# Kernel tuning notes

Measured on AMD Instinct MI355X. Metric: run time of the kernel, lower is better.

## Reference

```python
import jax, jax.numpy as jnp
import numpy as np

NEG_MAX = -jnp.finfo(jnp.float32).max


def apply_rotary(x):
    # x: (b, h, n, d) with d = key_dim; interleaved rotary (lucidrains rotary-embedding-torch)
    d = x.shape[-1]
    n = x.shape[-2]
    inv_freq = 1.0 / (10000.0 ** (jnp.arange(0, d, 2, dtype=jnp.float32) / d))
    t = jnp.arange(n, dtype=jnp.float32)
    freqs = t[:, None] * inv_freq[None, :]              # (n, d/2)
    cos, sin = jnp.cos(freqs), jnp.sin(freqs)
    x1, x2 = x[..., 0::2], x[..., 1::2]                 # even/odd interleaved pairs
    out1 = x1 * cos - x2 * sin
    out2 = x1 * sin + x2 * cos
    return jnp.stack([out1, out2], axis=-1).reshape(x.shape)


def setup_inputs() -> dict:
    key = jax.random.key(0)
    ks = jax.random.split(key, 12)
    b, n, dim, de = 2, 1024, 256, 64
    h, kd, vd = 8, 32, 32
    node_in = jax.random.normal(ks[0], (b, n, dim), dtype=jnp.float32)
    edge_in = jax.random.normal(ks[1], (b, n, n, de), dtype=jnp.float32)
    mask = jax.random.randint(ks[2], (b, n), 0, 2).astype(bool)
    s = 1.0 / np.sqrt(dim)
    Wq = jax.random.normal(ks[3], (dim, h * kd), dtype=jnp.float32) * s
    Wk = jax.random.normal(ks[4], (dim, h * kd), dtype=jnp.float32) * s
    Wv = jax.random.normal(ks[5], (dim, h * vd), dtype=jnp.float32) * s
    We = jax.random.normal(ks[6], (de, h), dtype=jnp.float32) * (1.0 / np.sqrt(de))
    be = jax.random.normal(ks[7], (h,), dtype=jnp.float32) * 0.01
    Wo = jax.random.normal(ks[8], (h * (vd + de), dim), dtype=jnp.float32) * (1.0 / np.sqrt(h * (vd + de)))
    bo = jax.random.normal(ks[9], (dim,), dtype=jnp.float32) * 0.01
    return {"node_in": node_in, "edge_in": edge_in, "mask": mask,
            "Wq": Wq, "Wk": Wk, "Wv": Wv, "We": We, "be": be, "Wo": Wo, "bo": bo}


def reference(node_in, edge_in, mask, Wq, Wk, Wv, We, be, Wo, bo):
    b, n, dim = node_in.shape
    h = be.shape[0]
    kd = Wq.shape[1] // h
    vd = Wv.shape[1] // h
    num_attn_logits = 2
    node_scale = (num_attn_logits * kd) ** -0.5
    edge_scale = num_attn_logits ** -0.5

    # projections -> (b, h, n, d)
    def proj(W, d):
        return (node_in @ W).reshape(b, n, h, d).transpose(0, 2, 1, 3)
    q, k, v = proj(Wq, kd), proj(Wk, kd), proj(Wv, vd)
    q, k = apply_rotary(q), apply_rotary(k)

    logits = jnp.einsum('bhid,bhjd->bhij', q, k) * node_scale
    edge_bias = (jnp.einsum('bijd,dh->bijh', edge_in, We) + be)  # (b, n, n, h)
    logits = logits + edge_bias.transpose(0, 3, 1, 2) * edge_scale

    pair_mask = mask[:, :, None] & mask[:, None, :]              # (b, n, n)
    logits = jnp.where(pair_mask[:, None, :, :], logits, NEG_MAX)

    attn = jax.nn.softmax(logits, axis=-1)                       # (b, h, n, n)

    res_node = jnp.einsum('bhij,bhjd->bhid', attn, v)            # (b, h, n, vd)
    res_edge = jnp.einsum('bhij,bijd->bhid', attn, edge_in)      # (b, h, n, de)

    res_node = res_node.transpose(0, 2, 1, 3).reshape(b, n, h * vd)
    res_edge = res_edge.transpose(0, 2, 1, 3).reshape(b, n, -1)
    out = jnp.concatenate([res_node, res_edge], axis=-1) @ Wo + bo
    return out
```

## Files before the change

kernel.cpp:

```cpp
#include <hip/hip_runtime.h>
#include <hip/hip_bf16.h>

typedef float f32x4 __attribute__((ext_vector_type(4)));
typedef short short8 __attribute__((ext_vector_type(8)));
typedef unsigned short u16;
typedef unsigned int u32;
typedef unsigned int u32x4 __attribute__((ext_vector_type(4)));
typedef unsigned short u16x8 __attribute__((ext_vector_type(8)));

#define NEG_MAX (-3.4028234663852886e38f)
#define NODE_SCALE 0.125f
#define EDGE_SCALE 0.70710678118654752f
#define TSTR 68
#define QSTR 36

__device__ __forceinline__ float bf2f(u16 u) {
  unsigned int w = ((unsigned int)u) << 16;
  return __builtin_bit_cast(float, w);
}
__device__ __forceinline__ u16 f2bf(float f) {
  unsigned int x = __builtin_bit_cast(unsigned int, f);
  x = x + 0x7FFFu + ((x >> 16) & 1u);
  return (u16)(x >> 16);
}
__device__ __forceinline__ float asf(u32 x) { return __builtin_bit_cast(float, x); }
__device__ __forceinline__ u32 cvtpk(float lo, float hi) {
  u32 r;
  asm("v_cvt_pk_bf16_f32 %0, %1, %2" : "=v"(r) : "v"(lo), "v"(hi));
  return r;
}

__global__ void mask_norm(const unsigned char* __restrict__ mraw,
                          float* __restrict__ mask_f) {
  __shared__ int flags;
  int t = threadIdx.x;
  if (t == 0) flags = 0;
  __syncthreads();
  const unsigned int* mu = (const unsigned int*)mraw;
  int f = 0;
  for (int e = t; e < 512; e += 256) { if (mu[e] > 1u) f |= 1; }
  for (int e = t; e < 2048; e += 256) { if (mraw[e] > 1) f |= 2; }
  if (f) atomicOr(&flags, f);
  __syncthreads();
  int fl = flags;
  for (int e = t; e < 2048; e += 256) {
    float v;
    if (!(fl & 1))      v = (mu[e] != 0u) ? 1.f : 0.f;
    else if (!(fl & 2)) v = (mraw[e] != 0) ? 1.f : 0.f;
    else                v = (((const float*)mraw)[e] != 0.f) ? 1.f : 0.f;
    mask_f[e] = v;
  }
}

__global__ __launch_bounds__(256) void qkv_rope(
    const float* __restrict__ node, const float* __restrict__ Wq,
    const float* __restrict__ Wk, const float* __restrict__ Wv,
    float* __restrict__ qw, u16* __restrict__ kwb, u16* __restrict__ vwb) {
  __shared__ __align__(16) float xs[8 * 256];
  int t = threadIdx.x;
  int row0 = blockIdx.x * 8;
#pragma unroll
  for (int p = 0; p < 2; ++p) {
    int f = p * 256 + t;
    *(f32x4*)(&xs[f * 4]) = *(const f32x4*)(node + (size_t)row0 * 256 + f * 4);
  }
  __syncthreads();
  float qa[8], ka[8], va[8];
#pragma unroll
  for (int r = 0; r < 8; ++r) { qa[r] = 0.f; ka[r] = 0.f; va[r] = 0.f; }
  for (int c = 0; c < 256; ++c) {
    float wq = Wq[c * 256 + t];
    float wk = Wk[c * 256 + t];
    float wv = Wv[c * 256 + t];
#pragma unroll
    for (int r = 0; r < 8; ++r) {
      float x = xs[r * 256 + c];
      qa[r] += x * wq; ka[r] += x * wk; va[r] += x * wv;
    }
  }
  int d = t & 31;
  float inv = powf(10000.f, -((float)(2 * (d >> 1)) * (1.f / 32.f)));
  int h = t >> 5;
#pragma unroll
  for (int r = 0; r < 8; ++r) {
    int gr = row0 + r;
    int b = gr >> 10, i = gr & 1023;
    float ang = (float)i * inv;
    float sn, cs;
    sincosf(ang, &sn, &cs);
    float qp = __shfl_xor(qa[r], 1, 64);
    float kp = __shfl_xor(ka[r], 1, 64);
    float qo = (d & 1) ? (qp * sn + qa[r] * cs) : (qa[r] * cs - qp * sn);
    float ko = (d & 1) ? (kp * sn + ka[r] * cs) : (ka[r] * cs - kp * sn);
    int idx = ((b * 8 + h) * 1024 + i) * 32 + d;
    qw[idx] = qo;
    kwb[idx] = f2bf(ko);
    vwb[idx] = f2bf(va[r]);
  }
}

#define WREG 1704
__global__ __launch_bounds__(256) void attn_fused(
    const float* __restrict__ edge, const float* __restrict__ qw,
    const u16* __restrict__ kwb, const u16* __restrict__ vwb,
    const float* __restrict__ We, const float* __restrict__ be,
    const float* __restrict__ mask_f, float* __restrict__ rescat) {
  __shared__ __align__(16) float S[4 * WREG];

  int bid = blockIdx.x;
  int xcd = bid & 7, slot = bid >> 3;
  int b = xcd >> 2;
  int i = (xcd & 3) * 256 + slot;
  int t = threadIdx.x;
  int lane = t & 63;
  int w = __builtin_amdgcn_readfirstlane(t >> 6);

  float* tile = S + w * WREG;
  float* Pf = tile + 1088;
  float* Bg = Pf + 160;
  float* qsw = Bg + 160;
  float* Rg = qsw + 288;

  int hg = lane >> 4, jl = lane & 15;
  int hD = lane >> 3, sD = lane & 7;
  int jrl = lane >> 2, c4 = lane & 3;
  int jh = sD >> 2, do4 = sD & 3;

  float mi = mask_f[b * 1024 + i];
  u32 mb = 0;
  if (mi != 0.f) {
#pragma unroll
    for (int tt = 0; tt < 16; ++tt) {
      float v = mask_f[b * 1024 + tt * 64 + w * 16 + jl];
      mb |= (v != 0.f ? 1u : 0u) << tt;
    }
  }
  float bes1 = be[hg] * EDGE_SCALE, bes2 = be[hg + 4] * EDGE_SCALE;

  {
    int qh = lane >> 3, qd = (lane & 7) * 4;
    f32x4 qv = *(const f32x4*)(qw + ((size_t)((b * 8 + qh) * 1024 + i)) * 32 + qd);
    *(f32x4*)(qsw + qh * QSTR + qd) = qv;
  }

  short8 weA0, weA1;
  {
    int hh = lane & 15, g = lane >> 4;
#pragma unroll
    for (int e = 0; e < 8; ++e) {
      int d0 = g * 8 + e;
      float w0 = (hh < 8) ? We[d0 * 8 + hh] * EDGE_SCALE : 0.f;
      float w1 = (hh < 8) ? We[(d0 + 32) * 8 + hh] * EDGE_SCALE : 0.f;
      weA0[e] = (short)f2bf(w0);
      weA1[e] = (short)f2bf(w1);
    }
  }

  const float* ebase = edge + ((size_t)(b * 1024 + i)) * (1024 * 64);
  const float* gsrc = ebase + (size_t)(w * 16 + jrl) * 64 + c4 * 16;
  float* wdst = tile + jrl * TSTR + c4 * 16;

  {
    f32x4 a0 = __builtin_nontemporal_load((const f32x4*)(gsrc + 0));
    f32x4 a1 = __builtin_nontemporal_load((const f32x4*)(gsrc + 4));
    f32x4 a2 = __builtin_nontemporal_load((const f32x4*)(gsrc + 8));
    f32x4 a3 = __builtin_nontemporal_load((const f32x4*)(gsrc + 12));
    *(f32x4*)(wdst + 0) = a0;
    *(f32x4*)(wdst + 4) = a1;
    *(f32x4*)(wdst + 8) = a2;
    *(f32x4*)(wdst + 12) = a3;
  }

  float m1 = NEG_MAX, m2 = NEG_MAX, s1 = 0.f, s2 = 0.f;
  f32x4 av0 = {0.f, 0.f, 0.f, 0.f}, av1 = {0.f, 0.f, 0.f, 0.f};
  f32x4 ae0 = {0.f, 0.f, 0.f, 0.f}, ae1 = {0.f, 0.f, 0.f, 0.f};

  for (int tt = 0; tt < 16; ++tt) {
    int j0 = tt * 64;
    bool pf = tt < 15;
    f32x4 st0, st1, st2, st3;
    if (pf) {
      const float* g = gsrc + (size_t)(j0 + 64) * 64;
      st0 = __builtin_nontemporal_load((const f32x4*)(g + 0));
      st1 = __builtin_nontemporal_load((const f32x4*)(g + 4));
      st2 = __builtin_nontemporal_load((const f32x4*)(g + 8));
      st3 = __builtin_nontemporal_load((const f32x4*)(g + 12));
    }
    int jg = j0 + w * 16 + jl;
    const u16* kr1 = kwb + ((size_t)((b * 8 + hg) * 1024 + jg)) * 32;
    const u16* kr2 = kwb + ((size_t)((b * 8 + hg + 4) * 1024 + jg)) * 32;
    u32x4 k1[4], k2[4];
#pragma unroll
    for (int g = 0; g < 4; ++g) {
      k1[g] = *(const u32x4*)(kr1 + g * 8);
      k2[g] = *(const u32x4*)(kr2 + g * 8);
    }
    {
      const float* rp = tile + jl * TSTR + hg * 8;
      f32x4 ea0 = *(const f32x4*)(rp + 0);
      f32x4 ea1 = *(const f32x4*)(rp + 4);
      f32x4 eb0 = *(const f32x4*)(rp + 32);
      f32x4 eb1 = *(const f32x4*)(rp + 36);
      u32x4 p0, p1;
      p0[0] = cvtpk(ea0.x, ea0.y); p0[1] = cvtpk(ea0.z, ea0.w);
      p0[2] = cvtpk(ea1.x, ea1.y); p0[3] = cvtpk(ea1.z, ea1.w);
      p1[0] = cvtpk(eb0.x, eb0.y); p1[1] = cvtpk(eb0.z, eb0.w);
      p1[2] = cvtpk(eb1.x, eb1.y); p1[3] = cvtpk(eb1.z, eb1.w);
      short8 bf0 = __builtin_bit_cast(short8, p0);
      short8 bf1 = __builtin_bit_cast(short8, p1);
      f32x4 bacc = {0.f, 0.f, 0.f, 0.f};
      bacc = __builtin_amdgcn_mfma_f32_16x16x32_bf16(weA0, bf0, bacc, 0, 0, 0);
      bacc = __builtin_amdgcn_mfma_f32_16x16x32_bf16(weA1, bf1, bacc, 0, 0, 0);
      if (lane < 32) {
        float* bg = Bg + hg * 80 + jl;
        bg[0] = bacc[0];
        bg[20] = bacc[1];
        bg[40] = bacc[2];
        bg[60] = bacc[3];
      }
    }
    float qk1 = 0.f, qk2 = 0.f;
    {
      const float* q1p = qsw + hg * QSTR;
      const float* q2p = qsw + (hg + 4) * QSTR;
#pragma unroll
      for (int g = 0; g < 4; ++g) {
        f32x4 q1a = *(const f32x4*)(q1p + g * 8);
        f32x4 q1b = *(const f32x4*)(q1p + g * 8 + 4);
        f32x4 q2a = *(const f32x4*)(q2p + g * 8);
        f32x4 q2b = *(const f32x4*)(q2p + g * 8 + 4);
        u32 ka0 = k1[g][0], ka1 = k1[g][1], ka2 = k1[g][2], ka3 = k1[g][3];
        u32 kb0 = k2[g][0], kb1 = k2[g][1], kb2 = k2[g][2], kb3 = k2[g][3];
        qk1 = fmaf(asf(ka0 << 16), q1a.x, qk1);
        qk1 = fmaf(asf(ka0 & 0xffff0000u), q1a.y, qk1);
        qk1 = fmaf(asf(ka1 << 16), q1a.z, qk1);
        qk1 = fmaf(asf(ka1 & 0xffff0000u), q1a.w, qk1);
        qk1 = fmaf(asf(ka2 << 16), q1b.x, qk1);
        qk1 = fmaf(asf(ka2 & 0xffff0000u), q1b.y, qk1);
        qk1 = fmaf(asf(ka3 << 16), q1b.z, qk1);
        qk1 = fmaf(asf(ka3 & 0xffff0000u), q1b.w, qk1);
        qk2 = fmaf(asf(kb0 << 16), q2a.x, qk2);
        qk2 = fmaf(asf(kb0 & 0xffff0000u), q2a.y, qk2);
        qk2 = fmaf(asf(kb1 << 16), q2a.z, qk2);
        qk2 = fmaf(asf(kb1 & 0xffff0000u), q2a.w, qk2);
        qk2 = fmaf(asf(kb2 << 16), q2b.x, qk2);
        qk2 = fmaf(asf(kb2 & 0xffff0000u), q2b.y, qk2);
        qk2 = fmaf(asf(kb3 << 16), q2b.z, qk2);
        qk2 = fmaf(asf(kb3 & 0xffff0000u), q2b.w, qk2);
      }
    }
    {
      float bias1 = Bg[hg * 20 + jl], bias2 = Bg[(hg + 4) * 20 + jl];
      bool pm = (mb >> tt) & 1u;
      float l1 = pm ? (NODE_SCALE * qk1 + bias1 + bes1) : NEG_MAX;
      float l2 = pm ? (NODE_SCALE * qk2 + bias2 + bes2) : NEG_MAX;
      float mx1 = l1, mx2 = l2;
#pragma unroll
      for (int off = 1; off < 16; off <<= 1) {
        mx1 = fmaxf(mx1, __shfl_xor(mx1, off, 64));
        mx2 = fmaxf(mx2, __shfl_xor(mx2, off, 64));
      }
      float mn1 = fmaxf(m1, mx1), mn2 = fmaxf(m2, mx2);
      float p1 = __expf(l1 - mn1), p2 = __expf(l2 - mn2);
      float ps1 = p1, ps2 = p2;
#pragma unroll
      for (int off = 1; off < 16; off <<= 1) {
        ps1 += __shfl_xor(ps1, off, 64);
        ps2 += __shfl_xor(ps2, off, 64);
      }
      float r1 = __expf(m1 - mn1), r2 = __expf(m2 - mn2);
      s1 = s1 * r1 + ps1; m1 = mn1;
      s2 = s2 * r2 + ps2; m2 = mn2;
      Pf[hg * 20 + jl] = p1;
      Pf[(hg + 4) * 20 + jl] = p2;
      if (jl == 0) { Rg[hg] = r1; Rg[hg + 4] = r2; }
    }
    {
      float r = Rg[hD];
      const float* prow = Pf + hD * 20;
      f32x4 pr0 = *(const f32x4*)(prow + 0);
      f32x4 pr1 = *(const f32x4*)(prow + 4);
      f32x4 pr2 = *(const f32x4*)(prow + 8);
      f32x4 pr3 = *(const f32x4*)(prow + 12);
      {
        const u16* vb = vwb + ((size_t)((b * 8 + hD) * 1024 + j0 + w * 16 + jh * 8)) * 32 + do4 * 8;
        f32x4 prA = jh ? pr2 : pr0, prB = jh ? pr3 : pr1;
        f32x4 sv0 = {0.f, 0.f, 0.f, 0.f}, sv1 = {0.f, 0.f, 0.f, 0.f};
#pragma unroll
        for (int x = 0; x < 8; ++x) {
          float p = (x < 4) ? prA[x] : prB[x - 4];
          u32x4 vv = *(const u32x4*)(vb + (size_t)x * 32);
          f32x4 e0 = {asf(vv[0] << 16), asf(vv[0] & 0xffff0000u),
                      asf(vv[1] << 16), asf(vv[1] & 0xffff0000u)};
          f32x4 e1 = {asf(vv[2] << 16), asf(vv[2] & 0xffff0000u),
                      asf(vv[3] << 16), asf(vv[3] & 0xffff0000u)};
          sv0 += e0 * p;
          sv1 += e1 * p;
        }
        av0 = av0 * r + sv0;
        av1 = av1 * r + sv1;
      }
      {
        const float* eB = tile + sD * 8;
        f32x4 se0 = {0.f, 0.f, 0.f, 0.f}, se1 = {0.f, 0.f, 0.f, 0.f};
#pragma unroll
        for (int x = 0; x < 16; ++x) {
          float p = (x < 4) ? pr0[x] : (x < 8) ? pr1[x - 4]
                  : (x < 12) ? pr2[x - 8] : pr3[x - 12];
          f32x4 e0 = *(const f32x4*)(eB + x * TSTR);
          f32x4 e1 = *(const f32x4*)(eB + x * TSTR + 4);
          se0 += e0 * p;
          se1 += e1 * p;
        }
        ae0 = ae0 * r + se0;
        ae1 = ae1 * r + se1;
      }
    }
    if (pf) {
      *(f32x4*)(wdst + 0) = st0;
      *(f32x4*)(wdst + 4) = st1;
      *(f32x4*)(wdst + 8) = st2;
      *(f32x4*)(wdst + 12) = st3;
    }
  }

  __syncthreads();
  float* mrg = S + w * 1040;
  if (jl == 0) {
    mrg[hg] = m1; mrg[hg + 4] = m2;
    mrg[8 + hg] = s1; mrg[8 + hg + 4] = s2;
  }
  *(f32x4*)(mrg + 16 + jh * 256 + hD * 32 + do4 * 8) = av0;
  *(f32x4*)(mrg + 16 + jh * 256 + hD * 32 + do4 * 8 + 4) = av1;
  *(f32x4*)(mrg + 528 + hD * 64 + sD * 8) = ae0;
  *(f32x4*)(mrg + 528 + hD * 64 + sD * 8 + 4) = ae1;
  __syncthreads();
  {
    int h = t >> 5, d = t & 31;
    float mx = fmaxf(fmaxf(S[h], S[1040 + h]), fmaxf(S[2080 + h], S[3120 + h]));
    float ew[4];
    float ssum = 0.f, vsum = 0.f;
#pragma unroll
    for (int ww = 0; ww < 4; ++ww) {
      const float* mw = S + ww * 1040;
      ew[ww] = __expf(mw[h] - mx);
      ssum += mw[8 + h] * ew[ww];
      vsum += (mw[16 + h * 32 + d] + mw[16 + 256 + h * 32 + d]) * ew[ww];
    }
    float inv = 1.f / ssum;
    size_t obase = ((size_t)(b * 1024 + i)) * 768;
    rescat[obase + h * 32 + d] = vsum * inv;
    float e0 = 0.f, e1 = 0.f;
#pragma unroll
    for (int ww = 0; ww < 4; ++ww) {
      const float* mw = S + ww * 1040;
      e0 += mw[528 + h * 64 + d] * ew[ww];
      e1 += mw[528 + h * 64 + 32 + d] * ew[ww];
    }
    rescat[obase + 256 + h * 64 + d] = e0 * inv;
    rescat[obase + 256 + h * 64 + 32 + d] = e1 * inv;
  }
}

__global__ __launch_bounds__(256) void out_proj(
    const float* __restrict__ rescat, const float* __restrict__ Wo,
    const float* __restrict__ bo, float* __restrict__ out) {
  __shared__ __align__(16) float xs[8 * 768];
  int t = threadIdx.x;
  int row0 = blockIdx.x * 8;
#pragma unroll
  for (int p = 0; p < 6; ++p) {
    int f = p * 256 + t;
    *(f32x4*)(&xs[f * 4]) = *(const f32x4*)(rescat + (size_t)row0 * 768 + f * 4);
  }
  __syncthreads();
  float acc[8];
#pragma unroll
  for (int r = 0; r < 8; ++r) acc[r] = 0.f;
  for (int c = 0; c < 768; ++c) {
    float w = Wo[c * 256 + t];
#pragma unroll
    for (int r = 0; r < 8; ++r) acc[r] += xs[r * 768 + c] * w;
  }
  float bias = bo[t];
#pragma unroll
  for (int r = 0; r < 8; ++r)
    out[(size_t)(row0 + r) * 256 + t] = acc[r] + bias;
}

extern "C" void kernel_launch(void* const* d_in, const int* in_sizes, int n_in,
                              void* d_out, int out_size, void* d_ws, size_t ws_size,
                              hipStream_t stream) {
  const float* node = (const float*)d_in[0];
  const float* edge = (const float*)d_in[1];
  const unsigned char* mask = (const unsigned char*)d_in[2];
  const float* Wq = (const float*)d_in[3];
  const float* Wk = (const float*)d_in[4];
  const float* Wv = (const float*)d_in[5];
  const float* We = (const float*)d_in[6];
  const float* be = (const float*)d_in[7];
  const float* Wo = (const float*)d_in[8];
  const float* bo = (const float*)d_in[9];

  float* ws = (float*)d_ws;
  float* qw = ws;
  u16* kwb = (u16*)(ws + 524288);
  u16* vwb = kwb + 524288;
  float* rescat = ws + 1048576;
  float* mask_f = ws + 2621440;

  hipLaunchKernelGGL(mask_norm, dim3(1), dim3(256), 0, stream, mask, mask_f);
  hipLaunchKernelGGL(qkv_rope, dim3(256), dim3(256), 0, stream,
                     node, Wq, Wk, Wv, qw, kwb, vwb);
  hipLaunchKernelGGL(attn_fused, dim3(2048), dim3(256), 0, stream,
                     edge, qw, kwb, vwb, We, be, mask_f, rescat);
  hipLaunchKernelGGL(out_proj, dim3(256), dim3(256), 0, stream,
                     rescat, Wo, bo, (float*)d_out);
}
```

Before: 395.5 us.

## Compute QK logits and P·edge aggregation with bf16 MFMA instead of scalar FMAs

Moves the per-tile Q·K dot products onto 16x16x32 bf16 MFMA. Q is pre-scaled, packed to bf16 and placed in one-hot per-head A fragments so the results accumulate into the same accumulator as the edge-bias MFMA. The P×edge reduction also becomes MFMA, with P and the edge tile converted to bf16 and the accumulators rescaled per head. This removes the scalar FMA loops and some LDS staging (Bg, qsw), shrinking the per-wave shared region. In exchange it rounds Q and P to bf16, and most lanes of the QK MFMAs multiply zeros.

```diff
diff --git a/kernel.cpp b/kernel.cpp
--- a/kernel.cpp
+++ b/kernel.cpp
@@ -6,18 +6,12 @@
 typedef unsigned short u16;
 typedef unsigned int u32;
 typedef unsigned int u32x4 __attribute__((ext_vector_type(4)));
-typedef unsigned short u16x8 __attribute__((ext_vector_type(8)));
 
 #define NEG_MAX (-3.4028234663852886e38f)
 #define NODE_SCALE 0.125f
 #define EDGE_SCALE 0.70710678118654752f
 #define TSTR 68
-#define QSTR 36
-
-__device__ __forceinline__ float bf2f(u16 u) {
-  unsigned int w = ((unsigned int)u) << 16;
-  return __builtin_bit_cast(float, w);
-}
+
 __device__ __forceinline__ u16 f2bf(float f) {
   unsigned int x = __builtin_bit_cast(unsigned int, f);
   x = x + 0x7FFFu + ((x >> 16) & 1u);
@@ -99,7 +93,7 @@
   }
 }
 
-#define WREG 1704
+#define WREG 1280
 __global__ __launch_bounds__(256) void attn_fused(
     const float* __restrict__ edge, const float* __restrict__ qw,
     const u16* __restrict__ kwb, const u16* __restrict__ vwb,
@@ -117,11 +111,10 @@
 
   float* tile = S + w * WREG;
   float* Pf = tile + 1088;
-  float* Bg = Pf + 160;
-  float* qsw = Bg + 160;
-  float* Rg = qsw + 288;
-
-  int hg = lane >> 4, jl = lane & 15;
+  float* Rg = tile + 1248;
+
+  int j16 = lane & 15;
+  int hq = lane >> 4;
   int hD = lane >> 3, sD = lane & 7;
   int jrl = lane >> 2, c4 = lane & 3;
   int jh = sD >> 2, do4 = sD & 3;
@@ -131,17 +124,12 @@
   if (mi != 0.f) {
 #pragma unroll
     for (int tt = 0; tt < 16; ++tt) {
-      float v = mask_f[b * 1024 + tt * 64 + w * 16 + jl];
+      float v = mask_f[b * 1024 + tt * 64 + w * 16 + j16];
       mb |= (v != 0.f ? 1u : 0u) << tt;
     }
   }
-  float bes1 = be[hg] * EDGE_SCALE, bes2 = be[hg + 4] * EDGE_SCALE;
-
-  {
-    int qh = lane >> 3, qd = (lane & 7) * 4;
-    f32x4 qv = *(const f32x4*)(qw + ((size_t)((b * 8 + qh) * 1024 + i)) * 32 + qd);
-    *(f32x4*)(qsw + qh * QSTR + qd) = qv;
-  }
+  f32x4 besq = *(const f32x4*)(be + (hq & 1) * 4);
+  besq *= EDGE_SCALE;
 
   short8 weA0, weA1;
   {
@@ -154,6 +142,23 @@
       weA0[e] = (short)f2bf(w0);
       weA1[e] = (short)f2bf(w1);
     }
+  }
+
+  short8 qA[8];
+  {
+    int hh = (lane & 15) & 7;
+    const float* qp = qw + ((size_t)((b * 8 + hh) * 1024 + i)) * 32 + (lane >> 4) * 8;
+    f32x4 qv0 = *(const f32x4*)(qp);
+    f32x4 qv1 = *(const f32x4*)(qp + 4);
+    qv0 *= NODE_SCALE;
+    qv1 *= NODE_SCALE;
+    u32x4 qpk;
+    qpk[0] = cvtpk(qv0.x, qv0.y); qpk[1] = cvtpk(qv0.z, qv0.w);
+    qpk[2] = cvtpk(qv1.x, qv1.y); qpk[3] = cvtpk(qv1.z, qv1.w);
+    u32x4 zz = {0u, 0u, 0u, 0u};
+#pragma unroll
+    for (int h = 0; h < 8; ++h)
+      qA[h] = __builtin_bit_cast(short8, ((lane & 15) == h) ? qpk : zz);
   }
 
   const float* ebase = edge + ((size_t)(b * 1024 + i)) * (1024 * 64);
@@ -171,9 +176,11 @@
     *(f32x4*)(wdst + 12) = a3;
   }
 
-  float m1 = NEG_MAX, m2 = NEG_MAX, s1 = 0.f, s2 = 0.f;
+  f32x4 vm = {NEG_MAX, NEG_MAX, NEG_MAX, NEG_MAX};
+  f32x4 vs = {0.f, 0.f, 0.f, 0.f};
   f32x4 av0 = {0.f, 0.f, 0.f, 0.f}, av1 = {0.f, 0.f, 0.f, 0.f};
-  f32x4 ae0 = {0.f, 0.f, 0.f, 0.f}, ae1 = {0.f, 0.f, 0.f, 0.f};
+  f32x4 acce0 = {0.f, 0.f, 0.f, 0.f}, acce1 = {0.f, 0.f, 0.f, 0.f};
+  f32x4 acce2 = {0.f, 0.f, 0.f, 0.f}, acce3 = {0.f, 0.f, 0.f, 0.f};
 
   for (int tt = 0; tt < 16; ++tt) {
     int j0 = tt * 64;
@@ -186,17 +193,10 @@
       st2 = __builtin_nontemporal_load((const f32x4*)(g + 8));
       st3 = __builtin_nontemporal_load((const f32x4*)(g + 12));
     }
-    int jg = j0 + w * 16 + jl;
-    const u16* kr1 = kwb + ((size_t)((b * 8 + hg) * 1024 + jg)) * 32;
-    const u16* kr2 = kwb + ((size_t)((b * 8 + hg + 4) * 1024 + jg)) * 32;
-    u32x4 k1[4], k2[4];
-#pragma unroll
-    for (int g = 0; g < 4; ++g) {
-      k1[g] = *(const u32x4*)(kr1 + g * 8);
-      k2[g] = *(const u32x4*)(kr2 + g * 8);
-    }
+
+    f32x4 bacc = {0.f, 0.f, 0.f, 0.f};
     {
-      const float* rp = tile + jl * TSTR + hg * 8;
+      const float* rp = tile + j16 * TSTR + hq * 8;
       f32x4 ea0 = *(const f32x4*)(rp + 0);
       f32x4 ea1 = *(const f32x4*)(rp + 4);
       f32x4 eb0 = *(const f32x4*)(rp + 32);
@@ -206,75 +206,53 @@
       p0[2] = cvtpk(ea1.x, ea1.y); p0[3] = cvtpk(ea1.z, ea1.w);
       p1[0] = cvtpk(eb0.x, eb0.y); p1[1] = cvtpk(eb0.z, eb0.w);
       p1[2] = cvtpk(eb1.x, eb1.y); p1[3] = cvtpk(eb1.z, eb1.w);
-      short8 bf0 = __builtin_bit_cast(short8, p0);
-      short8 bf1 = __builtin_bit_cast(short8, p1);
-      f32x4 bacc = {0.f, 0.f, 0.f, 0.f};
-      bacc = __builtin_amdgcn_mfma_f32_16x16x32_bf16(weA0, bf0, bacc, 0, 0, 0);
-      bacc = __builtin_amdgcn_mfma_f32_16x16x32_bf16(weA1, bf1, bacc, 0, 0, 0);
+      bacc = __builtin_amdgcn_mfma_f32_16x16x32_bf16(
+          weA0, __builtin_bit_cast(short8, p0), bacc, 0, 0, 0);
+      bacc = __builtin_amdgcn_mfma_f32_16x16x32_bf16(
+          weA1, __builtin_bit_cast(short8, p1), bacc, 0, 0, 0);
+    }
+#pragma unroll
+    for (int h = 0; h < 8; ++h) {
+      const u16* kp = kwb + ((size_t)((b * 8 + h) * 1024 + j0 + w * 16 + j16)) * 32 + hq * 8;
+      short8 kB = *(const short8*)kp;
+      bacc = __builtin_amdgcn_mfma_f32_16x16x32_bf16(qA[h], kB, bacc, 0, 0, 0);
+    }
+
+    f32x4 p;
+    {
+      bool pm = (mb >> tt) & 1u;
+      f32x4 l;
+#pragma unroll
+      for (int r = 0; r < 4; ++r) l[r] = pm ? (bacc[r] + besq[r]) : NEG_MAX;
+      f32x4 mx = l;
+#pragma unroll
+      for (int off = 1; off < 16; off <<= 1) {
+#pragma unroll
+        for (int r = 0; r < 4; ++r) mx[r] = fmaxf(mx[r], __shfl_xor(mx[r], off, 64));
+      }
+      f32x4 mn, rs;
+#pragma unroll
+      for (int r = 0; r < 4; ++r) {
+        mn[r] = fmaxf(vm[r], mx[r]);
+        p[r] = __expf(l[r] - mn[r]);
+      }
+      f32x4 ps = p;
+#pragma unroll
+      for (int off = 1; off < 16; off <<= 1) {
+#pragma unroll
+        for (int r = 0; r < 4; ++r) ps[r] += __shfl_xor(ps[r], off, 64);
+      }
+#pragma unroll
+      for (int r = 0; r < 4; ++r) rs[r] = __expf(vm[r] - mn[r]);
+      vs = vs * rs + ps;
+      vm = mn;
       if (lane < 32) {
-        float* bg = Bg + hg * 80 + jl;
-        bg[0] = bacc[0];
-        bg[20] = bacc[1];
-        bg[40] = bacc[2];
-        bg[60] = bacc[3];
+        float* pw = Pf + hq * 80 + j16;
+        pw[0] = p[0]; pw[20] = p[1]; pw[40] = p[2]; pw[60] = p[3];
+        if (j16 == 0) *(f32x4*)(Rg + hq * 4) = rs;
       }
     }
-    float qk1 = 0.f, qk2 = 0.f;
-    {
-      const float* q1p = qsw + hg * QSTR;
-      const float* q2p = qsw + (hg + 4) * QSTR;
-#pragma unroll
-      for (int g = 0; g < 4; ++g) {
-        f32x4 q1a = *(const f32x4*)(q1p + g * 8);
-        f32x4 q1b = *(const f32x4*)(q1p + g * 8 + 4);
-        f32x4 q2a = *(const f32x4*)(q2p + g * 8);
-        f32x4 q2b = *(const f32x4*)(q2p + g * 8 + 4);
-        u32 ka0 = k1[g][0], ka1 = k1[g][1], ka2 = k1[g][2], ka3 = k1[g][3];
-        u32 kb0 = k2[g][0], kb1 = k2[g][1], kb2 = k2[g][2], kb3 = k2[g][3];
-        qk1 = fmaf(asf(ka0 << 16), q1a.x, qk1);
-        qk1 = fmaf(asf(ka0 & 0xffff0000u), q1a.y, qk1);
-        qk1 = fmaf(asf(ka1 << 16), q1a.z, qk1);
-        qk1 = fmaf(asf(ka1 & 0xffff0000u), q1a.w, qk1);
-        qk1 = fmaf(asf(ka2 << 16), q1b.x, qk1);
-        qk1 = fmaf(asf(ka2 & 0xffff0000u), q1b.y, qk1);
-        qk1 = fmaf(asf(ka3 << 16), q1b.z, qk1);
-        qk1 = fmaf(asf(ka3 & 0xffff0000u), q1b.w, qk1);
-        qk2 = fmaf(asf(kb0 << 16), q2a.x, qk2);
-        qk2 = fmaf(asf(kb0 & 0xffff0000u), q2a.y, qk2);
-        qk2 = fmaf(asf(kb1 << 16), q2a.z, qk2);
-        qk2 = fmaf(asf(kb1 & 0xffff0000u), q2a.w, qk2);
-        qk2 = fmaf(asf(kb2 << 16), q2b.x, qk2);
-        qk2 = fmaf(asf(kb2 & 0xffff0000u), q2b.y, qk2);
-        qk2 = fmaf(asf(kb3 << 16), q2b.z, qk2);
-        qk2 = fmaf(asf(kb3 & 0xffff0000u), q2b.w, qk2);
-      }
-    }
-    {
-      float bias1 = Bg[hg * 20 + jl], bias2 = Bg[(hg + 4) * 20 + jl];
-      bool pm = (mb >> tt) & 1u;
-      float l1 = pm ? (NODE_SCALE * qk1 + bias1 + bes1) : NEG_MAX;
-      float l2 = pm ? (NODE_SCALE * qk2 + bias2 + bes2) : NEG_MAX;
-      float mx1 = l1, mx2 = l2;
-#pragma unroll
-      for (int off = 1; off < 16; off <<= 1) {
-        mx1 = fmaxf(mx1, __shfl_xor(mx1, off, 64));
-        mx2 = fmaxf(mx2, __shfl_xor(mx2, off, 64));
-      }
-      float mn1 = fmaxf(m1, mx1), mn2 = fmaxf(m2, mx2);
-      float p1 = __expf(l1 - mn1), p2 = __expf(l2 - mn2);
-      float ps1 = p1, ps2 = p2;
-#pragma unroll
-      for (int off = 1; off < 16; off <<= 1) {
-        ps1 += __shfl_xor(ps1, off, 64);
-        ps2 += __shfl_xor(ps2, off, 64);
-      }
-      float r1 = __expf(m1 - mn1), r2 = __expf(m2 - mn2);
-      s1 = s1 * r1 + ps1; m1 = mn1;
-      s2 = s2 * r2 + ps2; m2 = mn2;
-      Pf[hg * 20 + jl] = p1;
-      Pf[(hg + 4) * 20 + jl] = p2;
-      if (jl == 0) { Rg[hg] = r1; Rg[hg + 4] = r2; }
-    }
+
     {
       float r = Rg[hD];
       const float* prow = Pf + hD * 20;
@@ -282,40 +260,53 @@
       f32x4 pr1 = *(const f32x4*)(prow + 4);
       f32x4 pr2 = *(const f32x4*)(prow + 8);
       f32x4 pr3 = *(const f32x4*)(prow + 12);
-      {
-        const u16* vb = vwb + ((size_t)((b * 8 + hD) * 1024 + j0 + w * 16 + jh * 8)) * 32 + do4 * 8;
-        f32x4 prA = jh ? pr2 : pr0, prB = jh ? pr3 : pr1;
-        f32x4 sv0 = {0.f, 0.f, 0.f, 0.f}, sv1 = {0.f, 0.f, 0.f, 0.f};
-#pragma unroll
-        for (int x = 0; x < 8; ++x) {
-          float p = (x < 4) ? prA[x] : prB[x - 4];
-          u32x4 vv = *(const u32x4*)(vb + (size_t)x * 32);
-          f32x4 e0 = {asf(vv[0] << 16), asf(vv[0] & 0xffff0000u),
-                      asf(vv[1] << 16), asf(vv[1] & 0xffff0000u)};
-          f32x4 e1 = {asf(vv[2] << 16), asf(vv[2] & 0xffff0000u),
-                      asf(vv[3] << 16), asf(vv[3] & 0xffff0000u)};
-          sv0 += e0 * p;
-          sv1 += e1 * p;
-        }
-        av0 = av0 * r + sv0;
-        av1 = av1 * r + sv1;
+      const u16* vb = vwb + ((size_t)((b * 8 + hD) * 1024 + j0 + w * 16 + jh * 8)) * 32 + do4 * 8;
+      f32x4 prA = jh ? pr2 : pr0, prB = jh ? pr3 : pr1;
+      f32x4 sv0 = {0.f, 0.f, 0.f, 0.f}, sv1 = {0.f, 0.f, 0.f, 0.f};
+#pragma unroll
+      for (int x = 0; x < 8; ++x) {
+        float pv = (x < 4) ? prA[x] : prB[x - 4];
+        u32x4 vv = *(const u32x4*)(vb + (size_t)x * 32);
+        f32x4 e0 = {asf(vv[0] << 16), asf(vv[0] & 0xffff0000u),
+                    asf(vv[1] << 16), asf(vv[1] & 0xffff0000u)};
+        f32x4 e1 = {asf(vv[2] << 16), asf(vv[2] & 0xffff0000u),
+                    asf(vv[3] << 16), asf(vv[3] & 0xffff0000u)};
+        sv0 += e0 * pv;
+        sv1 += e1 * pv;
       }
-      {
-        const float* eB = tile + sD * 8;
-        f32x4 se0 = {0.f, 0.f, 0.f, 0.f}, se1 = {0.f, 0.f, 0.f, 0.f};
-#pragma unroll
-        for (int x = 0; x < 16; ++x) {
-          float p = (x < 4) ? pr0[x] : (x < 8) ? pr1[x - 4]
-                  : (x < 12) ? pr2[x - 8] : pr3[x - 12];
-          f32x4 e0 = *(const f32x4*)(eB + x * TSTR);
-          f32x4 e1 = *(const f32x4*)(eB + x * TSTR + 4);
-          se0 += e0 * p;
-          se1 += e1 * p;
-        }
-        ae0 = ae0 * r + se0;
-        ae1 = ae1 * r + se1;
-      }
-    }
+      av0 = av0 * r + sv0;
+      av1 = av1 * r + sv1;
+    }
+
+    {
+      f32x4 rgv = *(const f32x4*)(Rg + (hq & 1) * 4);
+      const float* pArow = Pf + (lane & 7) * 20 + (hq & 1) * 8;
+      f32x4 pa0 = *(const f32x4*)(pArow);
+      f32x4 pa1 = *(const f32x4*)(pArow + 4);
+      u32x4 apk;
+      apk[0] = cvtpk(pa0.x, pa0.y); apk[1] = cvtpk(pa0.z, pa0.w);
+      apk[2] = cvtpk(pa1.x, pa1.y); apk[3] = cvtpk(pa1.z, pa1.w);
+      if (hq >= 2) apk = (u32x4){0u, 0u, 0u, 0u};
+      short8 pAf = __builtin_bit_cast(short8, apk);
+      const float* cb = tile + (hq & 1) * 8 * TSTR + j16;
+#define PE_STEP(ACC, NT) {                                                   \
+      float b0 = cb[(NT)*16 + 0*TSTR], b1 = cb[(NT)*16 + 1*TSTR];            \
+      float b2 = cb[(NT)*16 + 2*TSTR], b3 = cb[(NT)*16 + 3*TSTR];            \
+      float b4 = cb[(NT)*16 + 4*TSTR], b5 = cb[(NT)*16 + 5*TSTR];            \
+      float b6 = cb[(NT)*16 + 6*TSTR], b7 = cb[(NT)*16 + 7*TSTR];            \
+      u32x4 bpk;                                                             \
+      bpk[0] = cvtpk(b0, b1); bpk[1] = cvtpk(b2, b3);                        \
+      bpk[2] = cvtpk(b4, b5); bpk[3] = cvtpk(b6, b7);                        \
+      ACC = ACC * rgv;                                                       \
+      ACC = __builtin_amdgcn_mfma_f32_16x16x32_bf16(                         \
+          pAf, __builtin_bit_cast(short8, bpk), ACC, 0, 0, 0); }
+      PE_STEP(acce0, 0)
+      PE_STEP(acce1, 1)
+      PE_STEP(acce2, 2)
+      PE_STEP(acce3, 3)
+#undef PE_STEP
+    }
+
     if (pf) {
       *(f32x4*)(wdst + 0) = st0;
       *(f32x4*)(wdst + 4) = st1;
@@ -326,14 +317,22 @@
 
   __syncthreads();
   float* mrg = S + w * 1040;
-  if (jl == 0) {
-    mrg[hg] = m1; mrg[hg + 4] = m2;
-    mrg[8 + hg] = s1; mrg[8 + hg + 4] = s2;
+  if (lane < 32) {
+    int h0 = hq * 4;
+    if (j16 == 0) {
+#pragma unroll
+      for (int r = 0; r < 4; ++r) { mrg[h0 + r] = vm[r]; mrg[8 + h0 + r] = vs[r]; }
+    }
+#pragma unroll
+    for (int r = 0; r < 4; ++r) {
+      mrg[528 + (h0 + r) * 64 + 0 + j16] = acce0[r];
+      mrg[528 + (h0 + r) * 64 + 16 + j16] = acce1[r];
+      mrg[528 + (h0 + r) * 64 + 32 + j16] = acce2[r];
+      mrg[528 + (h0 + r) * 64 + 48 + j16] = acce3[r];
+    }
   }
   *(f32x4*)(mrg + 16 + jh * 256 + hD * 32 + do4 * 8) = av0;
   *(f32x4*)(mrg + 16 + jh * 256 + hD * 32 + do4 * 8 + 4) = av1;
-  *(f32x4*)(mrg + 528 + hD * 64 + sD * 8) = ae0;
-  *(f32x4*)(mrg + 528 + hD * 64 + sD * 8 + 4) = ae1;
   __syncthreads();
   {
     int h = t >> 5, d = t & 31;
```

New measurement: 393.8 us. About the same (-0.4%).
